# Kernel tuning notes

Measured on AMD Instinct MI355X. Metric: run time of the kernel, lower is better.

The kernel has to match this reference:

```python
import jax, jax.numpy as jnp
import numpy as np

MODES = (16, 16)
EMBED_DIM = 64
NUM_HEADS = 8


def spectral_conv(x, w):
    """FNO-style spectral conv. x: [B,S,Ci,H,W]; w: [Ci,Co,mx,my,2] (real/imag)."""
    wc = w[..., 0] + 1j * w[..., 1]
    H, W = x.shape[-2], x.shape[-1]
    mx, my = wc.shape[2], wc.shape[3]
    xf = jnp.fft.rfft2(x)                                   # [B,S,Ci,H,W//2+1]
    of = jnp.einsum('bsixy,ioxy->bsoxy', xf[..., :mx, :my], wc)
    out_f = jnp.zeros(x.shape[:2] + (wc.shape[1], H, W // 2 + 1), dtype=of.dtype)
    out_f = out_f.at[..., :mx, :my].set(of)
    return jnp.fft.irfft2(out_f, s=(H, W))


def log_cpb_bias(n_sub_x, n_sub_y, w1, b1, w2):
    """Swin-v2-style log-spaced continuous position bias -> [heads, S, S]."""
    cx = jnp.arange(n_sub_x, dtype=jnp.float32)
    cy = jnp.arange(n_sub_y, dtype=jnp.float32)
    coords = jnp.stack(jnp.meshgrid(cx, cy, indexing='ij'), axis=-1).reshape(-1, 2)
    rel = coords[:, None, :] - coords[None, :, :]           # [S,S,2]
    rel = jnp.sign(rel) * jnp.log1p(jnp.abs(rel))
    h = jax.nn.relu(rel @ w1 + b1)                          # [S,S,hidden]
    bias = h @ w2                                           # [S,S,heads]
    return jnp.transpose(bias, (2, 0, 1))


def _unflatten(f, num_heads, embed_dim):
    # [B,S,h*d,H,W] -> [B,h,S,d,H,W]
    B, S = f.shape[0], f.shape[1]
    f = f.reshape(B, S, num_heads, embed_dim, f.shape[-2], f.shape[-1])
    return jnp.transpose(f, (0, 2, 1, 3, 4, 5))


def setup_inputs() -> dict:
    key = jax.random.key(0)
    ks = jax.random.split(key, 9)
    B, S, D, H, W = 2, 64, EMBED_DIM, 32, 32
    hd = NUM_HEADS * D
    mx, my = MODES
    scale = 0.02
    return {
        'seq': jax.random.normal(ks[0], (B, S, D, H, W), dtype=jnp.float32),
        'wq': scale * jax.random.normal(ks[1], (D, hd, mx, my, 2), dtype=jnp.float32),
        'wk': scale * jax.random.normal(ks[2], (D, hd, mx, my, 2), dtype=jnp.float32),
        'wv': scale * jax.random.normal(ks[3], (D, hd, mx, my, 2), dtype=jnp.float32),
        'wo': scale * jax.random.normal(ks[4], (hd, D, mx, my, 2), dtype=jnp.float32),
        'cpb_w1': scale * jax.random.normal(ks[5], (2, D), dtype=jnp.float32),
        'cpb_b1': jnp.zeros((D,), dtype=jnp.float32),
        'cpb_w2': scale * jax.random.normal(ks[6], (D, NUM_HEADS), dtype=jnp.float32),
        'n_sub_x': 8,
        'n_sub_y': 8,
    }


def reference(seq, wq, wk, wv, wo, cpb_w1, cpb_b1, cpb_w2, n_sub_x, n_sub_y):
    q = _unflatten(spectral_conv(seq, wq), NUM_HEADS, EMBED_DIM)  # [B,h,S,d,H,W]
    k = _unflatten(spectral_conv(seq, wk), NUM_HEADS, EMBED_DIM)
    v = _unflatten(spectral_conv(seq, wv), NUM_HEADS, EMBED_DIM)

    bias = log_cpb_bias(n_sub_x, n_sub_y, cpb_w1, cpb_b1, cpb_w2)  # [h,S,S]

    d, H, W = q.shape[-3], q.shape[-2], q.shape[-1]
    scale = 1.0 / jnp.sqrt(jnp.asarray(d * H * W, dtype=q.dtype))
    scores = jnp.einsum('bhqdxy,bhkdxy->bhqk', q, k) * scale + bias[None]
    attn = jax.nn.softmax(scores, axis=-1)
    sa = jnp.einsum('bhqk,bhkdxy->bhqdxy', attn, v)          # [B,h,S,d,H,W]

    # _flatten: [B,h,S,d,H,W] -> [B,S,h*d,H,W]
    sa = jnp.transpose(sa, (0, 2, 1, 3, 4, 5))
    B, S = sa.shape[0], sa.shape[1]
    sa = sa.reshape(B, S, NUM_HEADS * EMBED_DIM, H, W)
    return spectral_conv(sa, wo)
```

## Files before the change

kernel.cpp:

```cpp
#include <hip/hip_runtime.h>

#define TWO_PI 6.28318530717958647692f

#define NH 8
#define CH 128
#define NCH 2

#define OFF_XM   0ull
#define OFF_WTA  (OFF_XM + 8388608ull)
#define OFF_WTB  (OFF_WTA + 16777216ull)
#define OFF_PO   (OFF_WTB + 16777216ull)
#define OFF_ATTN (OFF_PO + 16777216ull)
#define WS_TOTAL (OFF_ATTN + 262144ull)

typedef short bf16x8 __attribute__((ext_vector_type(8)));
typedef float f32x4 __attribute__((ext_vector_type(4)));
#define MFMA_B16(a, b, c) __builtin_amdgcn_mfma_f32_16x16x32_bf16(a, b, c, 0, 0, 0)

#define G2L(g, l) __builtin_amdgcn_global_load_lds( \
    (const __attribute__((address_space(1))) void*)(g), \
    (__attribute__((address_space(3))) void*)(l), 16, 0, 0)

__device__ __forceinline__ float bl(unsigned u) { return __uint_as_float(u << 16); }
__device__ __forceinline__ unsigned short f2b(float f) {
    unsigned u = __float_as_uint(f);
    return (unsigned short)((u + 0x7fffu + ((u >> 16) & 1u)) >> 16);
}
__device__ __forceinline__ unsigned pack2(float lo, float hi) {
    return (unsigned)f2b(lo) | ((unsigned)f2b(hi) << 16);
}

__device__ __forceinline__ bf16x8 mkfrag(const unsigned* __restrict__ Wt, int co_l, int ri,
                                         int ci0, bool dc) {
    unsigned a0 = Wt[(ci0 + 0) * 64 + (co_l ^ (ci0 + 0))];
    unsigned a1 = Wt[(ci0 + 1) * 64 + (co_l ^ (ci0 + 1))];
    unsigned a2 = Wt[(ci0 + 2) * 64 + (co_l ^ (ci0 + 2))];
    unsigned a3 = Wt[(ci0 + 3) * 64 + (co_l ^ (ci0 + 3))];
    uint4 r;
    if (ri) {
        if (dc) { r.x = 0u; r.y = 0u; r.z = 0u; r.w = 0u; }
        else {
            r.x = (a0 >> 16) | (a0 << 16); r.y = (a1 >> 16) | (a1 << 16);
            r.z = (a2 >> 16) | (a2 << 16); r.w = (a3 >> 16) | (a3 << 16);
        }
    } else {
        r.x = a0 ^ 0x80000000u; r.y = a1 ^ 0x80000000u;
        r.z = a2 ^ 0x80000000u; r.w = a3 ^ 0x80000000u;
    }
    return __builtin_bit_cast(bf16x8, r);
}

__global__ __launch_bounds__(256) void k_transpose2(const float* __restrict__ srcA, unsigned* __restrict__ dstA, int kindA,
                                                    const float* __restrict__ srcB, unsigned* __restrict__ dstB, int kindB,
                                                    int m0) {
    const float* in = (blockIdx.z == 0) ? srcA : srcB;
    unsigned* outp = (blockIdx.z == 0) ? dstA : dstB;
    int kind = (blockIdx.z == 0) ? kindA : kindB;
    __shared__ unsigned T[16][65];
    int tid = threadIdx.x;
    int r0 = blockIdx.x * 64;
    int ci, h;
    if (kind == 2) { h = r0 >> 12; ci = (r0 >> 6) & 63; }
    else           { ci = r0 >> 9; h = (r0 >> 6) & 7; }
    int ml0 = blockIdx.y * 16;
    int u = (m0 + ml0) >> 4;
    const float4* in4 = (const float4*)in;
    float fac1 = (kind == 0) ? 1.41421356f : 1.f;
    float facu = (kind == 0) ? (u > 0 ? 0.70710678f : 1.f)
               : (kind == 1) ? (u > 0 ? 0.5f : 1.f) : 1.f;
    #pragma unroll
    for (int p = 0; p < 2; ++p) {
        int f = tid + p * 256;
        int row = f >> 3, mc2 = (f & 7) * 2;
        float4 v = in4[(size_t)(r0 + row) * 128 + ((m0 + ml0) >> 1) + (f & 7)];
        float fac0 = (mc2 > 0) ? fac1 : facu;
        T[mc2][row] = pack2(v.x * fac0, v.y * fac0);
        T[mc2 + 1][row] = pack2(v.z * fac1, v.w * fac1);
    }
    __syncthreads();
    #pragma unroll
    for (int p = 0; p < 4; ++p) {
        int f = tid + p * 256;
        int ml = f >> 6, co = f & 63;
        outp[((size_t)((ml0 + ml) * 8 + h) << 12) + ci * 64 + (co ^ ci)] = T[ml][co];
    }
}

__global__ __launch_bounds__(256) void k_rfft_y(const float* __restrict__ seq,
                                                float2* __restrict__ T) {
    __shared__ float c32[32], s32[32];
    __shared__ float fld[32][33];
    int tid = threadIdx.x;
    int bc = blockIdx.x;
    if (tid < 32) { float s, c; __sincosf(TWO_PI * tid / 32.0f, &s, &c); c32[tid] = c; s32[tid] = s; }
    float4 v = ((const float4*)(seq + (size_t)bc * 1024))[tid];
    int x = tid >> 3, y4 = (tid & 7) * 4;
    fld[x][y4] = v.x; fld[x][y4 + 1] = v.y; fld[x][y4 + 2] = v.z; fld[x][y4 + 3] = v.w;
    __syncthreads();
    float2* op = T + (size_t)bc * 512;
    #pragma unroll
    for (int p = 0; p < 2; ++p) {
        int e = tid + p * 256;
        int xx = e >> 4, vv = e & 15;
        float sr = 0.f, si = 0.f;
        #pragma unroll
        for (int y = 0; y < 32; ++y) {
            float f = fld[xx][y];
            int ph = (vv * y) & 31;
            sr = fmaf(f, c32[ph], sr);
            si = fmaf(-f, s32[ph], si);
        }
        float2 t; t.x = sr; t.y = si;
        op[e] = t;
    }
}

__global__ __launch_bounds__(256) void k_rfft_x(const float2* __restrict__ T,
                                                unsigned short* __restrict__ XM) {
    __shared__ float c32[32], s32[32];
    __shared__ float2 t[8][512];
    int tid = threadIdx.x;
    int cig = blockIdx.x;
    int bs = blockIdx.y;
    if (tid < 32) { float s, c; __sincosf(TWO_PI * tid / 32.0f, &s, &c); c32[tid] = c; s32[tid] = s; }
    const float4* src = (const float4*)(T + ((size_t)bs * 64 + cig * 8) * 512);
    #pragma unroll
    for (int p = 0; p < 8; ++p) {
        int idx = tid + p * 256;
        float4 w = src[idx];
        int ch = idx >> 8, r2 = idx & 255;
        float2 t0; t0.x = w.x; t0.y = w.y;
        float2 t1; t1.x = w.z; t1.y = w.w;
        t[ch][r2 * 2] = t0; t[ch][r2 * 2 + 1] = t1;
    }
    __syncthreads();
    int u = tid >> 4, vv = tid & 15;
    unsigned outw[8];
    for (int ch = 0; ch < 8; ++ch) {
        float xr = 0.f, xi = 0.f;
        #pragma unroll
        for (int x = 0; x < 32; ++x) {
            float2 tv = t[ch][x * 16 + vv];
            int ph = (u * x) & 31;
            float c = c32[ph], s = s32[ph];
            xr += tv.x * c + tv.y * s;
            xi += tv.y * c - tv.x * s;
        }
        outw[ch] = pack2(xr, xi);
    }
    unsigned short* rowp = XM + ((size_t)tid * 128 + bs) * 128;
    uint4 a, b;
    a.x = outw[0]; a.y = outw[1]; a.z = outw[2]; a.w = outw[3];
    b.x = outw[4]; b.y = outw[5]; b.z = outw[6]; b.w = outw[7];
    int sw = bs & 7;
    *(uint4*)(rowp + ((cig * 2) ^ sw) * 8) = a;
    *(uint4*)(rowp + ((cig * 2 + 1) ^ sw) * 8) = b;
}

__global__ __launch_bounds__(512) void k_qks(const unsigned short* __restrict__ XM,
                                             const unsigned* __restrict__ WQ,
                                             const unsigned* __restrict__ WK,
                                             float* __restrict__ part, int mbase) {
    __shared__ __align__(16) unsigned char Xs[16384];
    __shared__ __align__(16) unsigned Wq[4096];
    __shared__ __align__(16) unsigned Wk[4096];
    unsigned char* Qs = Xs;
    unsigned char* Ks = (unsigned char*)Wq;
    int tid = threadIdx.x;
    int mg = blockIdx.x, h = blockIdx.y, b = blockIdx.z;
    int lane = tid & 63, w = tid >> 6;
    int lr = lane & 15, lg = lane >> 4;
    int wr = w & 1, wc = w >> 1;
    int sxa = (lr & 7) << 4;
    int ri = lr & 1;
    f32x4 zf = {0.f, 0.f, 0.f, 0.f};
    f32x4 sacc[2];
    sacc[0] = zf; sacc[1] = zf;
    for (int mm = 0; mm < 4; ++mm) {
        int ml = mg * 4 + mm;
        int mode = mbase + ml;
        bool dc = (mode == 0);
        __syncthreads();
        {
            const char* xg = (const char*)(XM + ((size_t)mode * 128 + b * 64) * 128);
            const char* tq = (const char*)(WQ + ((size_t)(ml * 8 + h) << 12));
            const char* tk = (const char*)(WK + ((size_t)(ml * 8 + h) << 12));
            #pragma unroll
            for (int p = 0; p < 2; ++p) {
                int off = (tid + p * 512) * 16;
                G2L(xg + off, Xs + off);
                G2L(tq + off, (char*)Wq + off);
                G2L(tk + off, (char*)Wk + off);
            }
        }
        __syncthreads();
        f32x4 qa[2][2], ka[2][2];
        {
            #pragma unroll
            for (int m = 0; m < 2; ++m)
                #pragma unroll
                for (int n = 0; n < 2; ++n) { qa[m][n] = zf; ka[m][n] = zf; }
            #pragma unroll
            for (int ks = 0; ks < 4; ++ks) {
                int kb = (ks * 64 + lg * 16) ^ sxa;
                int ci0 = ks * 16 + lg * 4;
                bf16x8 a0 = *(const bf16x8*)(Xs + (wr * 32 + lr) * 256 + kb);
                bf16x8 a1 = *(const bf16x8*)(Xs + (wr * 32 + 16 + lr) * 256 + kb);
                #pragma unroll
                for (int n = 0; n < 2; ++n) {
                    int co_l = wc * 16 + n * 8 + (lr >> 1);
                    bf16x8 bq = mkfrag(Wq, co_l, ri, ci0, dc);
                    bf16x8 bk = mkfrag(Wk, co_l, ri, ci0, dc);
                    qa[0][n] = MFMA_B16(a0, bq, qa[0][n]);
                    qa[1][n] = MFMA_B16(a1, bq, qa[1][n]);
                    ka[0][n] = MFMA_B16(a0, bk, ka[0][n]);
                    ka[1][n] = MFMA_B16(a1, bk, ka[1][n]);
                }
            }
        }
        __syncthreads();
        {
            #pragma unroll
            for (int m = 0; m < 2; ++m)
                #pragma unroll
                for (int n = 0; n < 2; ++n) {
                    int colb = (wc * 32 + n * 16 + lr) * 2;
                    #pragma unroll
                    for (int r = 0; r < 4; ++r) {
                        int row = wr * 32 + m * 16 + lg * 4 + r;
                        int swz = (row & 7) << 4;
                        *(unsigned short*)(Qs + row * 256 + (colb ^ swz)) = f2b(qa[m][n][r]);
                        *(unsigned short*)(Ks + row * 256 + (colb ^ swz)) = f2b(ka[m][n][r]);
                    }
                }
        }
        __syncthreads();
        {
            #pragma unroll
            for (int ks = 0; ks < 4; ++ks) {
                int kb = (ks * 64 + lg * 16) ^ sxa;
                bf16x8 a0 = *(const bf16x8*)(Qs + (wr * 32 + lr) * 256 + kb);
                bf16x8 a1 = *(const bf16x8*)(Qs + (wr * 32 + 16 + lr) * 256 + kb);
                bf16x8 b0 = *(const bf16x8*)(Ks + (wc * 16 + lr) * 256 + kb);
                sacc[0] = MFMA_B16(a0, b0, sacc[0]);
                sacc[1] = MFMA_B16(a1, b0, sacc[1]);
            }
        }
    }
    float* pp = part + (((size_t)((mbase >> 2) + mg) * 16 + b * 8 + h) << 12);
    #pragma unroll
    for (int m = 0; m < 2; ++m)
        #pragma unroll
        for (int r = 0; r < 4; ++r)
            pp[(wr * 32 + m * 16 + lg * 4 + r) * 64 + wc * 16 + lr] = sacc[m][r];
}

__global__ void k_softmax(const float* __restrict__ part,
                          const float* __restrict__ w1, const float* __restrict__ b1,
                          const float* __restrict__ w2, unsigned short* __restrict__ attnb) {
    int j = threadIdx.x;
    int i = blockIdx.x;
    int bh = blockIdx.y;
    int h = bh & 7;
    float s = 0.f;
    for (int mg = 0; mg < 64; ++mg)
        s += part[(((size_t)mg * 16 + bh) * 64 + i) * 64 + j];
    float dx = (float)((i >> 3) - (j >> 3));
    float dy = (float)((i & 7) - (j & 7));
    float rx = (dx > 0.f ? 1.f : (dx < 0.f ? -1.f : 0.f)) * log1pf(fabsf(dx));
    float ry = (dy > 0.f ? 1.f : (dy < 0.f ? -1.f : 0.f)) * log1pf(fabsf(dy));
    float bias = 0.f;
    for (int l = 0; l < 64; ++l) {
        float hv = fmaxf(rx * w1[l] + ry * w1[64 + l] + b1[l], 0.f);
        bias = fmaf(hv, w2[l * NH + h], bias);
    }
    s = s * (1.0f / 262144.0f) + bias;
    float m = s;
    for (int o = 32; o >= 1; o >>= 1) m = fmaxf(m, __shfl_xor(m, o));
    float e = expf(s - m);
    float t = e;
    for (int o = 32; o >= 1; o >>= 1) t += __shfl_xor(t, o);
    attnb[((size_t)bh * 64 + i) * 64 + j] = f2b(e / t);
}

__global__ __launch_bounds__(512) void k_savo(const unsigned short* __restrict__ XM,
                                              const unsigned* __restrict__ WV,
                                              const unsigned* __restrict__ WO,
                                              const unsigned short* __restrict__ attnb,
                                              float* __restrict__ outf, int mbase) {
    __shared__ __align__(16) unsigned char Xs[16384];
    __shared__ __align__(16) unsigned Wv[4096];
    __shared__ __align__(16) unsigned Wo[4096];
    unsigned char* Vt = (unsigned char*)Wv;
    unsigned char* Ss = (unsigned char*)Wv;
    int tid = threadIdx.x;
    int ml = blockIdx.x, b = blockIdx.y;
    int mode = mbase + ml;
    bool dc = (mode == 0);
    int lane = tid & 63, w = tid >> 6;
    int lr = lane & 15, lg = lane >> 4;
    int wr = w & 1, wc = w >> 1;
    int sxa = (lr & 7) << 4;
    int ri = lr & 1;
    f32x4 zf = {0.f, 0.f, 0.f, 0.f};
    {
        const char* xg = (const char*)(XM + ((size_t)mode * 128 + b * 64) * 128);
        #pragma unroll
        for (int p = 0; p < 2; ++p) {
            int off = (tid + p * 512) * 16;
            G2L(xg + off, Xs + off);
        }
    }
    f32x4 oacc[2][2];
    oacc[0][0] = zf; oacc[0][1] = zf; oacc[1][0] = zf; oacc[1][1] = zf;
    for (int h = 0; h < NH; ++h) {
        __syncthreads();
        {
            const char* tv = (const char*)(WV + ((size_t)(ml * 8 + h) << 12));
            const char* to = (const char*)(WO + ((size_t)(ml * 8 + h) << 12));
            #pragma unroll
            for (int p = 0; p < 2; ++p) {
                int off = (tid + p * 512) * 16;
                G2L(tv + off, (char*)Wv + off);
                G2L(to + off, (char*)Wo + off);
            }
        }
        bf16x8 af[2][2];
        #pragma unroll
        for (int m = 0; m < 2; ++m)
            #pragma unroll
            for (int ks = 0; ks < 2; ++ks) {
                int irow = wr * 32 + m * 16 + lr;
                af[m][ks] = *(const bf16x8*)(attnb + (((size_t)(b * 8 + h) * 64 + irow) * 64 + ks * 32 + lg * 8));
            }
        __syncthreads();
        f32x4 va[2][2];
        {
            va[0][0] = zf; va[0][1] = zf; va[1][0] = zf; va[1][1] = zf;
            #pragma unroll
            for (int ks = 0; ks < 4; ++ks) {
                int kb = (ks * 64 + lg * 16) ^ sxa;
                int ci0 = ks * 16 + lg * 4;
                bf16x8 a0 = *(const bf16x8*)(Xs + (wr * 32 + lr) * 256 + kb);
                bf16x8 a1 = *(const bf16x8*)(Xs + (wr * 32 + 16 + lr) * 256 + kb);
                #pragma unroll
                for (int n = 0; n < 2; ++n) {
                    int co_l = wc * 16 + n * 8 + (lr >> 1);
                    bf16x8 bb = mkfrag(Wv, co_l, ri, ci0, dc);
                    va[0][n] = MFMA_B16(a0, bb, va[0][n]);
                    va[1][n] = MFMA_B16(a1, bb, va[1][n]);
                }
            }
        }
        __syncthreads();
        {
            #pragma unroll
            for (int m = 0; m < 2; ++m)
                #pragma unroll
                for (int n = 0; n < 2; ++n) {
                    int cp = wc * 32 + n * 16 + lr;
                    int j0 = wr * 32 + m * 16 + lg * 4;
                    uint2 t;
                    t.x = pack2(va[m][n][0], va[m][n][1]);
                    t.y = pack2(va[m][n][2], va[m][n][3]);
                    *(uint2*)(Vt + cp * 128 + ((j0 * 2) ^ ((cp & 7) << 4))) = t;
                }
        }
        __syncthreads();
        f32x4 sa_[2][2];
        {
            sa_[0][0] = zf; sa_[0][1] = zf; sa_[1][0] = zf; sa_[1][1] = zf;
            #pragma unroll
            for (int ks = 0; ks < 2; ++ks) {
                #pragma unroll
                for (int n = 0; n < 2; ++n) {
                    int cp = wc * 32 + n * 16 + lr;
                    bf16x8 bb = *(const bf16x8*)(Vt + cp * 128 + ((ks * 64 + lg * 16) ^ ((cp & 7) << 4)));
                    sa_[0][n] = MFMA_B16(af[0][ks], bb, sa_[0][n]);
                    sa_[1][n] = MFMA_B16(af[1][ks], bb, sa_[1][n]);
                }
            }
        }
        __syncthreads();
        {
            #pragma unroll
            for (int m = 0; m < 2; ++m)
                #pragma unroll
                for (int n = 0; n < 2; ++n) {
                    int colb = (wc * 32 + n * 16 + lr) * 2;
                    #pragma unroll
                    for (int r = 0; r < 4; ++r) {
                        int row = wr * 32 + m * 16 + lg * 4 + r;
                        *(unsigned short*)(Ss + row * 256 + (colb ^ ((row & 7) << 4))) = f2b(sa_[m][n][r]);
                    }
                }
        }
        __syncthreads();
        {
            #pragma unroll
            for (int ks = 0; ks < 4; ++ks) {
                int kb = (ks * 64 + lg * 16) ^ sxa;
                int ci0 = ks * 16 + lg * 4;
                bf16x8 a0 = *(const bf16x8*)(Ss + (wr * 32 + lr) * 256 + kb);
                bf16x8 a1 = *(const bf16x8*)(Ss + (wr * 32 + 16 + lr) * 256 + kb);
                #pragma unroll
                for (int n = 0; n < 2; ++n) {
                    int co_l = wc * 16 + n * 8 + (lr >> 1);
                    bf16x8 bb = mkfrag(Wo, co_l, ri, ci0, false);
                    oacc[0][n] = MFMA_B16(a0, bb, oacc[0][n]);
                    oacc[1][n] = MFMA_B16(a1, bb, oacc[1][n]);
                }
            }
        }
    }
    #pragma unroll
    for (int m = 0; m < 2; ++m)
        #pragma unroll
        for (int n = 0; n < 2; ++n)
            #pragma unroll
            for (int r = 0; r < 4; ++r) {
                int i = wr * 32 + m * 16 + lg * 4 + r;
                int c2p = wc * 32 + n * 16 + lr;
                outf[((size_t)mode * 128 + b * 64 + i) * 128 + c2p] = oacc[m][n][r];
            }
}

__global__ __launch_bounds__(256) void k_irfft_v(const float* __restrict__ outf,
                                                 float2* __restrict__ G) {
    __shared__ float c32[32], s32[32];
    __shared__ float2 mf[256][8];
    int tid = threadIdx.x;
    int cg = blockIdx.x;
    int bs = blockIdx.y;
    if (tid < 32) { float s, c; __sincosf(TWO_PI * tid / 32.0f, &s, &c); c32[tid] = c; s32[tid] = s; }
    #pragma unroll
    for (int p = 0; p < 4; ++p) {
        int idx = tid + p * 256;
        int mode = idx >> 2, q = idx & 3;
        float4 v = *(const float4*)(outf + ((size_t)mode * 128 + bs) * 128 + cg * 16 + q * 4);
        float2 t0; t0.x = v.x; t0.y = v.y;
        float2 t1; t1.x = v.z; t1.y = v.w;
        mf[mode][q * 2] = t0; mf[mode][q * 2 + 1] = t1;
    }
    __syncthreads();
    #pragma unroll 1
    for (int p = 0; p < 2; ++p) {
        int e = tid + p * 256;
        int u = e >> 5, y = e & 31;
        #pragma unroll 1
        for (int ch = 0; ch < 8; ++ch) {
            float2 f0 = mf[u * 16][ch];
            float fr0 = f0.x;
            float fi0 = (u == 0) ? 0.f : f0.y;
            float ssr = 0.5f * fr0, ssi = 0.5f * fi0;
            #pragma unroll
            for (int v = 1; v < 16; ++v) {
                float2 f = mf[u * 16 + v][ch];
                int ph = (v * y) & 31;
                float c = c32[ph], s = s32[ph];
                ssr += f.x * c - f.y * s;
                ssi += f.x * s + f.y * c;
            }
            float2 g; g.x = ssr; g.y = ssi;
            G[(((size_t)u * 128 + bs) * 64 + cg * 8 + ch) * 32 + y] = g;
        }
    }
}

__global__ __launch_bounds__(256) void k_irfft_u(const float2* __restrict__ G,
                                                 float* __restrict__ out) {
    __shared__ float c32[32], s32[32];
    __shared__ float2 Gs[16][8][32];
    int tid = threadIdx.x;
    int cg = blockIdx.x;
    int bs = blockIdx.y;
    if (tid < 32) { float s, c; __sincosf(TWO_PI * tid / 32.0f, &s, &c); c32[tid] = c; s32[tid] = s; }
    #pragma unroll
    for (int p = 0; p < 8; ++p) {
        int idx = tid + p * 256;
        int y2 = idx & 15, ch = (idx >> 4) & 7, u = idx >> 7;
        float4 v = *(const float4*)((const float*)G + ((((size_t)u * 128 + bs) * 64 + cg * 8 + ch) * 32 + y2 * 2) * 2);
        float2 t0; t0.x = v.x; t0.y = v.y;
        float2 t1; t1.x = v.z; t1.y = v.w;
        Gs[u][ch][y2 * 2] = t0; Gs[u][ch][y2 * 2 + 1] = t1;
    }
    __syncthreads();
    #pragma unroll 1
    for (int p = 0; p < 4; ++p) {
        int pos = tid + p * 256;
        int x = pos >> 5, y = pos & 31;
        #pragma unroll 1
        for (int ch = 0; ch < 8; ++ch) {
            float acc = 0.f;
            #pragma unroll
            for (int u = 0; u < 16; ++u) {
                float2 g = Gs[u][ch][y];
                int ph = (u * x) & 31;
                acc += g.x * c32[ph] - g.y * s32[ph];
            }
            out[((size_t)(bs * 64 + cg * 8 + ch)) * 1024 + x * 32 + y] = acc * (1.0f / 512.0f);
        }
    }
}

extern "C" void kernel_launch(void* const* d_in, const int* in_sizes, int n_in,
                              void* d_out, int out_size, void* d_ws, size_t ws_size,
                              hipStream_t stream) {
    (void)in_sizes; (void)n_in; (void)out_size;
    const float* seq = (const float*)d_in[0];
    const float* wq = (const float*)d_in[1];
    const float* wk = (const float*)d_in[2];
    const float* wv = (const float*)d_in[3];
    const float* wo = (const float*)d_in[4];
    const float* cw1 = (const float*)d_in[5];
    const float* cb1 = (const float*)d_in[6];
    const float* cw2 = (const float*)d_in[7];
    float* out = (float*)d_out;
    char* ws = (char*)d_ws;
    if (ws_size < WS_TOTAL) return;

    unsigned short* XM = (unsigned short*)(ws + OFF_XM);
    unsigned* WTA = (unsigned*)(ws + OFF_WTA);
    unsigned* WTB = (unsigned*)(ws + OFF_WTB);
    float2* Tbuf = (float2*)(ws + OFF_WTA);
    float2* G = (float2*)(ws + OFF_WTA);
    float* PART = (float*)(ws + OFF_PO);
    float* OUTF = (float*)(ws + OFF_PO);
    unsigned short* ATTNB = (unsigned short*)(ws + OFF_ATTN);

    k_rfft_y<<<dim3(8192), dim3(256), 0, stream>>>(seq, Tbuf);
    k_rfft_x<<<dim3(8, 128), dim3(256), 0, stream>>>(Tbuf, XM);

    for (int c = 0; c < NCH; ++c) {
        int m0 = c * CH;
        k_transpose2<<<dim3(512, CH / 16, 2), dim3(256), 0, stream>>>(wq, WTA, 0, wk, WTB, 0, m0);
        k_qks<<<dim3(CH / 4, NH, 2), dim3(512), 0, stream>>>(XM, WTA, WTB, PART, m0);
    }
    k_softmax<<<dim3(64, 16), dim3(64), 0, stream>>>(PART, cw1, cb1, cw2, ATTNB);

    for (int c = 0; c < NCH; ++c) {
        int m0 = c * CH;
        k_transpose2<<<dim3(512, CH / 16, 2), dim3(256), 0, stream>>>(wv, WTA, 1, wo, WTB, 2, m0);
        k_savo<<<dim3(CH, 2), dim3(512), 0, stream>>>(XM, WTA, WTB, ATTNB, OUTF, m0);
    }
    k_irfft_v<<<dim3(8, 128), dim3(256), 0, stream>>>(OUTF, G);
    k_irfft_u<<<dim3(8, 128), dim3(256), 0, stream>>>(G, out);
}
```

Measured before the change: 321.1 us.

## Merge both batch items into one 1024-thread block to share weight tiles

The q/k score kernel and the attention/output kernel now process both batch elements in one 1024-thread block instead of separate blocks per batch. Each per-mode weight tile is loaded into LDS once and used by both halves, which halves weight traffic from global memory. In exchange the grid has half as many blocks, LDS per block grows (an extra 16KB buffer in k_savo), and larger blocks may lower occupancy and make barriers more costly.

```diff
diff --git a/kernel.cpp b/kernel.cpp
--- a/kernel.cpp
+++ b/kernel.cpp
@@ -157,22 +157,24 @@
     *(uint4*)(rowp + ((cig * 2 + 1) ^ sw) * 8) = b;
 }
 
-__global__ __launch_bounds__(512) void k_qks(const unsigned short* __restrict__ XM,
-                                             const unsigned* __restrict__ WQ,
-                                             const unsigned* __restrict__ WK,
-                                             float* __restrict__ part, int mbase) {
-    __shared__ __align__(16) unsigned char Xs[16384];
+__global__ __launch_bounds__(1024) void k_qks(const unsigned short* __restrict__ XM,
+                                              const unsigned* __restrict__ WQ,
+                                              const unsigned* __restrict__ WK,
+                                              float* __restrict__ part, int mbase) {
+    __shared__ __align__(16) unsigned char Xs[32768];
     __shared__ __align__(16) unsigned Wq[4096];
     __shared__ __align__(16) unsigned Wk[4096];
-    unsigned char* Qs = Xs;
-    unsigned char* Ks = (unsigned char*)Wq;
-    int tid = threadIdx.x;
-    int mg = blockIdx.x, h = blockIdx.y, b = blockIdx.z;
+    int tid = threadIdx.x;
+    int mg = blockIdx.x, h = blockIdx.y;
     int lane = tid & 63, w = tid >> 6;
+    int bsel = w >> 3;
+    int w8 = w & 7;
     int lr = lane & 15, lg = lane >> 4;
-    int wr = w & 1, wc = w >> 1;
+    int wr = w8 & 1, wc = w8 >> 1;
     int sxa = (lr & 7) << 4;
     int ri = lr & 1;
+    int rb = bsel * 64;
+    unsigned char* Kbase = bsel ? (unsigned char*)Wk : (unsigned char*)Wq;
     f32x4 zf = {0.f, 0.f, 0.f, 0.f};
     f32x4 sacc[2];
     sacc[0] = zf; sacc[1] = zf;
@@ -182,16 +184,14 @@
         bool dc = (mode == 0);
         __syncthreads();
         {
-            const char* xg = (const char*)(XM + ((size_t)mode * 128 + b * 64) * 128);
+            const char* xg = (const char*)(XM + (size_t)mode * 128 * 128);
             const char* tq = (const char*)(WQ + ((size_t)(ml * 8 + h) << 12));
             const char* tk = (const char*)(WK + ((size_t)(ml * 8 + h) << 12));
-            #pragma unroll
-            for (int p = 0; p < 2; ++p) {
-                int off = (tid + p * 512) * 16;
-                G2L(xg + off, Xs + off);
-                G2L(tq + off, (char*)Wq + off);
-                G2L(tk + off, (char*)Wk + off);
-            }
+            int off = tid * 16;
+            G2L(xg + off, Xs + off);
+            G2L(xg + 16384 + off, Xs + 16384 + off);
+            G2L(tq + off, (char*)Wq + off);
+            G2L(tk + off, (char*)Wk + off);
         }
         __syncthreads();
         f32x4 qa[2][2], ka[2][2];
@@ -204,8 +204,8 @@
             for (int ks = 0; ks < 4; ++ks) {
                 int kb = (ks * 64 + lg * 16) ^ sxa;
                 int ci0 = ks * 16 + lg * 4;
-                bf16x8 a0 = *(const bf16x8*)(Xs + (wr * 32 + lr) * 256 + kb);
-                bf16x8 a1 = *(const bf16x8*)(Xs + (wr * 32 + 16 + lr) * 256 + kb);
+                bf16x8 a0 = *(const bf16x8*)(Xs + (rb + wr * 32 + lr) * 256 + kb);
+                bf16x8 a1 = *(const bf16x8*)(Xs + (rb + wr * 32 + 16 + lr) * 256 + kb);
                 #pragma unroll
                 for (int n = 0; n < 2; ++n) {
                     int co_l = wc * 16 + n * 8 + (lr >> 1);
@@ -227,10 +227,10 @@
                     int colb = (wc * 32 + n * 16 + lr) * 2;
                     #pragma unroll
                     for (int r = 0; r < 4; ++r) {
-                        int row = wr * 32 + m * 16 + lg * 4 + r;
-                        int swz = (row & 7) << 4;
-                        *(unsigned short*)(Qs + row * 256 + (colb ^ swz)) = f2b(qa[m][n][r]);
-                        *(unsigned short*)(Ks + row * 256 + (colb ^ swz)) = f2b(ka[m][n][r]);
+                        int rl = wr * 32 + m * 16 + lg * 4 + r;
+                        int swz = (rl & 7) << 4;
+                        *(unsigned short*)(Xs + (rb + rl) * 256 + (colb ^ swz)) = f2b(qa[m][n][r]);
+                        *(unsigned short*)(Kbase + rl * 256 + (colb ^ swz)) = f2b(ka[m][n][r]);
                     }
                 }
         }
@@ -239,15 +239,15 @@
             #pragma unroll
             for (int ks = 0; ks < 4; ++ks) {
                 int kb = (ks * 64 + lg * 16) ^ sxa;
-                bf16x8 a0 = *(const bf16x8*)(Qs + (wr * 32 + lr) * 256 + kb);
-                bf16x8 a1 = *(const bf16x8*)(Qs + (wr * 32 + 16 + lr) * 256 + kb);
-                bf16x8 b0 = *(const bf16x8*)(Ks + (wc * 16 + lr) * 256 + kb);
+                bf16x8 a0 = *(const bf16x8*)(Xs + (rb + wr * 32 + lr) * 256 + kb);
+                bf16x8 a1 = *(const bf16x8*)(Xs + (rb + wr * 32 + 16 + lr) * 256 + kb);
+                bf16x8 b0 = *(const bf16x8*)(Kbase + (wc * 16 + lr) * 256 + kb);
                 sacc[0] = MFMA_B16(a0, b0, sacc[0]);
                 sacc[1] = MFMA_B16(a1, b0, sacc[1]);
             }
         }
     }
-    float* pp = part + (((size_t)((mbase >> 2) + mg) * 16 + b * 8 + h) << 12);
+    float* pp = part + (((size_t)((mbase >> 2) + mg) * 16 + bsel * 8 + h) << 12);
     #pragma unroll
     for (int m = 0; m < 2; ++m)
         #pragma unroll
@@ -283,33 +283,34 @@
     attnb[((size_t)bh * 64 + i) * 64 + j] = f2b(e / t);
 }
 
-__global__ __launch_bounds__(512) void k_savo(const unsigned short* __restrict__ XM,
-                                              const unsigned* __restrict__ WV,
-                                              const unsigned* __restrict__ WO,
-                                              const unsigned short* __restrict__ attnb,
-                                              float* __restrict__ outf, int mbase) {
-    __shared__ __align__(16) unsigned char Xs[16384];
+__global__ __launch_bounds__(1024) void k_savo(const unsigned short* __restrict__ XM,
+                                               const unsigned* __restrict__ WV,
+                                               const unsigned* __restrict__ WO,
+                                               const unsigned short* __restrict__ attnb,
+                                               float* __restrict__ outf, int mbase) {
+    __shared__ __align__(16) unsigned char Xs[32768];
     __shared__ __align__(16) unsigned Wv[4096];
     __shared__ __align__(16) unsigned Wo[4096];
-    unsigned char* Vt = (unsigned char*)Wv;
-    unsigned char* Ss = (unsigned char*)Wv;
-    int tid = threadIdx.x;
-    int ml = blockIdx.x, b = blockIdx.y;
+    __shared__ __align__(16) unsigned char Vt1[16384];
+    int tid = threadIdx.x;
+    int ml = blockIdx.x;
     int mode = mbase + ml;
     bool dc = (mode == 0);
     int lane = tid & 63, w = tid >> 6;
+    int bsel = w >> 3;
+    int w8 = w & 7;
     int lr = lane & 15, lg = lane >> 4;
-    int wr = w & 1, wc = w >> 1;
+    int wr = w8 & 1, wc = w8 >> 1;
     int sxa = (lr & 7) << 4;
     int ri = lr & 1;
+    int rb = bsel * 64;
+    unsigned char* Vtb = bsel ? Vt1 : (unsigned char*)Wv;
     f32x4 zf = {0.f, 0.f, 0.f, 0.f};
     {
-        const char* xg = (const char*)(XM + ((size_t)mode * 128 + b * 64) * 128);
-        #pragma unroll
-        for (int p = 0; p < 2; ++p) {
-            int off = (tid + p * 512) * 16;
-            G2L(xg + off, Xs + off);
-        }
+        const char* xg = (const char*)(XM + (size_t)mode * 128 * 128);
+        int off = tid * 16;
+        G2L(xg + off, Xs + off);
+        G2L(xg + 16384 + off, Xs + 16384 + off);
     }
     f32x4 oacc[2][2];
     oacc[0][0] = zf; oacc[0][1] = zf; oacc[1][0] = zf; oacc[1][1] = zf;
@@ -318,12 +319,9 @@
         {
             const char* tv = (const char*)(WV + ((size_t)(ml * 8 + h) << 12));
             const char* to = (const char*)(WO + ((size_t)(ml * 8 + h) << 12));
-            #pragma unroll
-            for (int p = 0; p < 2; ++p) {
-                int off = (tid + p * 512) * 16;
-                G2L(tv + off, (char*)Wv + off);
-                G2L(to + off, (char*)Wo + off);
-            }
+            int off = tid * 16;
+            G2L(tv + off, (char*)Wv + off);
+            G2L(to + off, (char*)Wo + off);
         }
         bf16x8 af[2][2];
         #pragma unroll
@@ -331,7 +329,7 @@
             #pragma unroll
             for (int ks = 0; ks < 2; ++ks) {
                 int irow = wr * 32 + m * 16 + lr;
-                af[m][ks] = *(const bf16x8*)(attnb + (((size_t)(b * 8 + h) * 64 + irow) * 64 + ks * 32 + lg * 8));
+                af[m][ks] = *(const bf16x8*)(attnb + (((size_t)(bsel * 8 + h) * 64 + irow) * 64 + ks * 32 + lg * 8));
             }
         __syncthreads();
         f32x4 va[2][2];
@@ -341,8 +339,8 @@
             for (int ks = 0; ks < 4; ++ks) {
                 int kb = (ks * 64 + lg * 16) ^ sxa;
                 int ci0 = ks * 16 + lg * 4;
-                bf16x8 a0 = *(const bf16x8*)(Xs + (wr * 32 + lr) * 256 + kb);
-                bf16x8 a1 = *(const bf16x8*)(Xs + (wr * 32 + 16 + lr) * 256 + kb);
+                bf16x8 a0 = *(const bf16x8*)(Xs + (rb + wr * 32 + lr) * 256 + kb);
+                bf16x8 a1 = *(const bf16x8*)(Xs + (rb + wr * 32 + 16 + lr) * 256 + kb);
                 #pragma unroll
                 for (int n = 0; n < 2; ++n) {
                     int co_l = wc * 16 + n * 8 + (lr >> 1);
@@ -363,7 +361,7 @@
                     uint2 t;
                     t.x = pack2(va[m][n][0], va[m][n][1]);
                     t.y = pack2(va[m][n][2], va[m][n][3]);
-                    *(uint2*)(Vt + cp * 128 + ((j0 * 2) ^ ((cp & 7) << 4))) = t;
+                    *(uint2*)(Vtb + cp * 128 + ((j0 * 2) ^ ((cp & 7) << 4))) = t;
                 }
         }
         __syncthreads();
@@ -375,7 +373,7 @@
                 #pragma unroll
                 for (int n = 0; n < 2; ++n) {
                     int cp = wc * 32 + n * 16 + lr;
-                    bf16x8 bb = *(const bf16x8*)(Vt + cp * 128 + ((ks * 64 + lg * 16) ^ ((cp & 7) << 4)));
+                    bf16x8 bb = *(const bf16x8*)(Vtb + cp * 128 + ((ks * 64 + lg * 16) ^ ((cp & 7) << 4)));
                     sa_[0][n] = MFMA_B16(af[0][ks], bb, sa_[0][n]);
                     sa_[1][n] = MFMA_B16(af[1][ks], bb, sa_[1][n]);
                 }
@@ -390,8 +388,8 @@
                     int colb = (wc * 32 + n * 16 + lr) * 2;
                     #pragma unroll
                     for (int r = 0; r < 4; ++r) {
-                        int row = wr * 32 + m * 16 + lg * 4 + r;
-                        *(unsigned short*)(Ss + row * 256 + (colb ^ ((row & 7) << 4))) = f2b(sa_[m][n][r]);
+                        int rl = wr * 32 + m * 16 + lg * 4 + r;
+                        *(unsigned short*)(Vtb + rl * 256 + (colb ^ ((rl & 7) << 4))) = f2b(sa_[m][n][r]);
                     }
                 }
         }
@@ -401,8 +399,8 @@
             for (int ks = 0; ks < 4; ++ks) {
                 int kb = (ks * 64 + lg * 16) ^ sxa;
                 int ci0 = ks * 16 + lg * 4;
-                bf16x8 a0 = *(const bf16x8*)(Ss + (wr * 32 + lr) * 256 + kb);
-                bf16x8 a1 = *(const bf16x8*)(Ss + (wr * 32 + 16 + lr) * 256 + kb);
+                bf16x8 a0 = *(const bf16x8*)(Vtb + (wr * 32 + lr) * 256 + kb);
+                bf16x8 a1 = *(const bf16x8*)(Vtb + (wr * 32 + 16 + lr) * 256 + kb);
                 #pragma unroll
                 for (int n = 0; n < 2; ++n) {
                     int co_l = wc * 16 + n * 8 + (lr >> 1);
@@ -421,7 +419,7 @@
             for (int r = 0; r < 4; ++r) {
                 int i = wr * 32 + m * 16 + lg * 4 + r;
                 int c2p = wc * 32 + n * 16 + lr;
-                outf[((size_t)mode * 128 + b * 64 + i) * 128 + c2p] = oacc[m][n][r];
+                outf[((size_t)mode * 128 + rb + i) * 128 + c2p] = oacc[m][n][r];
             }
 }
 
@@ -534,14 +532,14 @@
     for (int c = 0; c < NCH; ++c) {
         int m0 = c * CH;
         k_transpose2<<<dim3(512, CH / 16, 2), dim3(256), 0, stream>>>(wq, WTA, 0, wk, WTB, 0, m0);
-        k_qks<<<dim3(CH / 4, NH, 2), dim3(512), 0, stream>>>(XM, WTA, WTB, PART, m0);
+        k_qks<<<dim3(CH / 4, NH), dim3(1024), 0, stream>>>(XM, WTA, WTB, PART, m0);
     }
     k_softmax<<<dim3(64, 16), dim3(64), 0, stream>>>(PART, cw1, cb1, cw2, ATTNB);
 
     for (int c = 0; c < NCH; ++c) {
         int m0 = c * CH;
         k_transpose2<<<dim3(512, CH / 16, 2), dim3(256), 0, stream>>>(wv, WTA, 1, wo, WTB, 2, m0);
-        k_savo<<<dim3(CH, 2), dim3(512), 0, stream>>>(XM, WTA, WTB, ATTNB, OUTF, m0);
+        k_savo<<<dim3(CH), dim3(1024), 0, stream>>>(XM, WTA, WTB, ATTNB, OUTF, m0);
     }
     k_irfft_v<<<dim3(8, 128), dim3(256), 0, stream>>>(OUTF, G);
     k_irfft_u<<<dim3(8, 128), dim3(256), 0, stream>>>(G, out);
```

New measurement: 531.9 us. 1.66x slower.
